# Performance work log

Measured on AMD Instinct MI355X. Metric: run time of the kernel, lower is better.

Reference implementation:

```python
import jax, jax.numpy as jnp
import numpy as np

N_NODES = 200_000
N_EDGES = 6_400_000
N_GRAPHS = 512


def _sage_conv(x, edge_index, Wl, bl, Wr):
    """PyG SAGEConv (mean aggr): lin_l(mean_j x_j) + lin_r(x_i).
    lin_l has bias, lin_r does not. Messages flow src -> dst."""
    src, dst = edge_index[0], edge_index[1]
    n = x.shape[0]
    # gather neighbor features [E, F] and segment-mean into dst nodes
    msg_sum = jax.ops.segment_sum(x[src], dst, num_segments=n)
    deg = jax.ops.segment_sum(jnp.ones((src.shape[0],), x.dtype), dst, num_segments=n)
    mean = msg_sum / jnp.maximum(deg, 1.0)[:, None]  # zero in-degree -> 0
    return mean @ Wl.T + bl + x @ Wr.T


def setup_inputs() -> dict:
    key = jax.random.key(0)
    ks = jax.random.split(key, 9)
    x = jax.random.normal(ks[0], (N_NODES, 1), dtype=jnp.float32)
    edge_index = jax.random.randint(ks[1], (2, N_EDGES), 0, N_NODES, dtype=jnp.int64)
    batch = jnp.sort(jax.random.randint(ks[2], (N_NODES,), 0, N_GRAPHS, dtype=jnp.int64))
    W1l = jax.random.normal(ks[3], (16, 1), dtype=jnp.float32)
    b1 = jax.random.normal(ks[4], (16,), dtype=jnp.float32)
    W1r = jax.random.normal(ks[5], (16, 1), dtype=jnp.float32)
    W2l = jax.random.normal(ks[6], (1, 16), dtype=jnp.float32)
    b2 = jax.random.normal(ks[7], (1,), dtype=jnp.float32)
    W2r = jax.random.normal(ks[8], (1, 16), dtype=jnp.float32)
    return {"x": x, "edge_index": edge_index, "batch": batch, "batch_size": N_GRAPHS,
            "W1l": W1l, "b1": b1, "W1r": W1r, "W2l": W2l, "b2": b2, "W2r": W2r}


def reference(x, edge_index, batch, batch_size, W1l, b1, W1r, W2l, b2, W2r):
    h = _sage_conv(x, edge_index, W1l, b1, W1r)          # [N, 16]
    h = jax.nn.relu(h)
    h = _sage_conv(h, edge_index, W2l, b2, W2r)          # [N, 1]
    # global_add_pool: segment-sum node features by graph id
    out = jax.ops.segment_sum(h, batch, num_segments=batch_size)  # [B, 1]
    return out
```

## Files before the change

### kernel.cpp

```cpp
#include <hip/hip_runtime.h>


#define BLK       1024
#define TILE      (BLK * 4)
#define NBLK      512
#define RING      64
#define NSB       25
#define SBSH      13
#define WMSK      8191u
#define OVFCAP    (1u << 20)
#define CNT_ONE   (1u << 25)
#define FX_BIAS   131072
#define SCALE     4096.0f
#define INV_SCALE (1.0f / 4096.0f)
#define IDQ       8388608.0f

__global__ __launch_bounds__(BLK) void partition_kernel(
    const int* __restrict__ ei, const float* __restrict__ x,
    unsigned* __restrict__ xq1, unsigned* __restrict__ pairs,
    unsigned* __restrict__ blockCnt, unsigned long long* __restrict__ ovf,
    unsigned* __restrict__ ovfTail, int E, int N, int bins, unsigned Mdiv,
    int nc) {
    extern __shared__ unsigned buf[];
    __shared__ unsigned cnt[512];
    const int tid = threadIdx.x;
    const unsigned bid = blockIdx.x;
    for (int j = tid; j < nc; j += BLK) cnt[j] = 0;

    for (int n = (int)bid * BLK + tid; n < N; n += NBLK * BLK)
        xq1[n] = CNT_ONE + (unsigned)((int)rintf(x[n] * SCALE) + FX_BIAS);
    __syncthreads();

    const int ntiles = (E + TILE - 1) / TILE;
    for (int t = (int)bid; t < ntiles; t += NBLK) {
        int e0 = t * TILE + tid * 4;
        int nv = E - e0; nv = nv < 0 ? 0 : (nv > 4 ? 4 : nv);
        int srcv[4], dstv[4];
        if (nv == 4 && ((E & 3) == 0)) {
            int4 s = *(const int4*)(ei + e0);
            int4 d = *(const int4*)(ei + E + e0);
            srcv[0] = s.x; srcv[1] = s.y; srcv[2] = s.z; srcv[3] = s.w;
            dstv[0] = d.x; dstv[1] = d.y; dstv[2] = d.z; dstv[3] = d.w;
        } else {
            for (int j = 0; j < nv; ++j) { srcv[j] = ei[e0 + j]; dstv[j] = ei[E + e0 + j]; }
        }
        for (int j = 0; j < 4; ++j) {
            if (j < nv) {
                unsigned dst = (unsigned)dstv[j];
                unsigned src = (unsigned)srcv[j];
                unsigned pt = (unsigned)(((unsigned long long)dst * Mdiv) >> 32);
                int ld = (int)dst - (int)pt * bins;
                while (ld >= bins) { ld -= bins; ++pt; }
                while (ld < 0)     { ld += bins; --pt; }
                unsigned cell = pt * NSB + (src >> SBSH);
                unsigned w = ((src & WMSK) << 14) | (unsigned)ld;
                unsigned idx = atomicAdd(&cnt[cell], 1u);
                if (idx < RING) {
                    buf[cell * RING + idx] = w;
                } else {
                    unsigned ot = atomicAdd(ovfTail, 1u);
                    if (ot < OVFCAP)
                        ovf[ot] = ((unsigned long long)cell << 32) | w;
                }
            }
        }
    }
    __syncthreads();
    {
        int wv6 = tid >> 6, lane = tid & 63;
        for (int r = wv6; r < nc; r += 16) {
            unsigned len = cnt[r]; if (len > RING) len = RING;
            unsigned* dp = pairs + ((((size_t)r << 9) | bid) << 6);
            for (unsigned jj = lane; jj < len; jj += 64)
                dp[jj] = buf[r * RING + jj];
            if (lane == 0) blockCnt[((size_t)r << 9) | bid] = len;
        }
    }
}

__global__ __launch_bounds__(BLK, 8) void bin1_kernel(
    const unsigned* __restrict__ pairs, const unsigned* __restrict__ blockCnt,
    const unsigned long long* __restrict__ ovf,
    const unsigned* __restrict__ ovfTail,
    const unsigned* __restrict__ xq1, unsigned* __restrict__ slab,
    int N, int bins) {
    extern __shared__ unsigned sm[];
    unsigned* xs = sm;
    unsigned* sb = sm + 8192;
    __shared__ unsigned scnt[NBLK];
    const int tid = threadIdx.x;
    const int cell = blockIdx.x;
    const int p = cell / NSB;
    const int sbk = cell - p * NSB;
    const int wb = sbk << SBSH;
    int nn = N - wb; if (nn > 8192) nn = 8192;
    for (int j = tid; j < nn; j += BLK) xs[j] = xq1[wb + j];
    for (int j = tid; j < bins; j += BLK) sb[j] = 0;
    for (int j = tid; j < NBLK; j += BLK) scnt[j] = blockCnt[((size_t)cell << 9) + j];
    __syncthreads();
    {
        int wv6 = tid >> 6, lane = tid & 63;
        for (int s = wv6; s < NBLK; s += 16) {
            int len = (int)scnt[s];
            const unsigned* sp = pairs + ((((size_t)cell << 9) | (unsigned)s) << 6);
            for (int jj = lane; jj < len; jj += 64) {
                unsigned w = sp[jj];
                atomicAdd(&sb[w & 16383u], xs[w >> 14]);
            }
        }
    }
    {
        unsigned ot = *ovfTail; if (ot > OVFCAP) ot = OVFCAP;
        for (unsigned e = tid; e < ot; e += BLK) {
            unsigned long long pk = ovf[e];
            if ((unsigned)(pk >> 32) == (unsigned)cell) {
                unsigned w = (unsigned)pk;
                atomicAdd(&sb[w & 16383u], xs[w >> 14]);
            }
        }
    }
    __syncthreads();
    unsigned* dst = slab + (size_t)sbk * N + (size_t)p * bins;
    int nb = N - p * bins; if (nb > bins) nb = bins;
    for (int j = tid; j < nb; j += BLK) dst[j] = sb[j];
}

__global__ void node_pass1_kernel(const float* __restrict__ x,
                                  const unsigned* __restrict__ slab,
                                  const float* __restrict__ W1l,
                                  const float* __restrict__ b1,
                                  const float* __restrict__ W1r,
                                  const float* __restrict__ W2l,
                                  const float* __restrict__ W2r,
                                  const float* __restrict__ b2,
                                  const int* __restrict__ batch,
                                  int* __restrict__ pvq,
                                  unsigned* __restrict__ zd,
                                  float* __restrict__ out,
                                  int N) {
    __shared__ float s_w1l[16], s_b1[16], s_w1r[16], s_w2l[16], s_w2r[16];
    if (threadIdx.x < 16) {
        s_w1l[threadIdx.x] = W1l[threadIdx.x];
        s_b1[threadIdx.x]  = b1[threadIdx.x];
        s_w1r[threadIdx.x] = W1r[threadIdx.x];
        s_w2l[threadIdx.x] = W2l[threadIdx.x];
        s_w2r[threadIdx.x] = W2r[threadIdx.x];
    }
    __syncthreads();
    int n = blockIdx.x * blockDim.x + threadIdx.x;
    float b2v = b2[0];
    float val = 0.0f;
    int g;
    if (n < N) {
        unsigned cnt = 0, fx = 0;
#pragma unroll
        for (int c = 0; c < NSB; ++c) {
            unsigned w = slab[(size_t)c * N + n];
            cnt += w >> 25;
            fx  += w & (CNT_ONE - 1);
        }
        float dg  = (float)cnt;
        float sum = (float)(int)(fx - cnt * (unsigned)FX_BIAS) * INV_SCALE;
        float m   = sum / fmaxf(dg, 1.0f);

        float xv = x[n];
        float pa = 0.0f, qa = 0.0f;
#pragma unroll
        for (int f = 0; f < 16; ++f) {
            float h = fmaf(m, s_w1l[f], fmaf(xv, s_w1r[f], s_b1[f]));
            h = fmaxf(h, 0.0f);
            pa = fmaf(h, s_w2l[f], pa);
            qa = fmaf(h, s_w2r[f], qa);
        }
        pvq[n] = (int)rintf(pa * SCALE);
        float invd = 1.0f / fmaxf(dg, 1.0f);
        unsigned q = (unsigned)rintf(invd * IDQ);
        if (q > 8388607u) q = 8388607u;
        g = batch[n];
        zd[n] = ((unsigned)g << 23) | q;
        val = qa + b2v;
    } else {
        g = batch[N - 1];
    }
    int g0 = __shfl(g, 0);
    unsigned long long same = __ballot(g == g0);
    if (same == ~0ULL) {
        for (int off = 32; off > 0; off >>= 1) val += __shfl_down(val, off);
        if ((threadIdx.x & 63) == 0) atomicAdd(&out[g0], val);
    } else {
        atomicAdd(&out[g], val);
    }
}

__global__ __launch_bounds__(BLK, 8) void pool_kernel(
    const unsigned* __restrict__ pairs, const unsigned* __restrict__ blockCnt,
    const unsigned long long* __restrict__ ovf,
    const unsigned* __restrict__ ovfTail,
    const int* __restrict__ pvq, const unsigned* __restrict__ zd,
    unsigned long long* __restrict__ outq,
    int N, int bins) {
    extern __shared__ unsigned sm[];
    int* ps = (int*)sm;
    unsigned* zs = sm + 8192;
    unsigned long long* gbin =
        (unsigned long long*)(sm + 8192 + 10000);
    __shared__ unsigned scnt[NBLK];
    const int tid = threadIdx.x;
    const int cell = blockIdx.x;
    const int p = cell / NSB;
    const int sbk = cell - p * NSB;
    const int wb = sbk << SBSH;
    int nn = N - wb; if (nn > 8192) nn = 8192;
    for (int j = tid; j < nn; j += BLK) ps[j] = pvq[wb + j];
    int nb = N - p * bins; if (nb > bins) nb = bins;
    for (int j = tid; j < nb; j += BLK) zs[j] = zd[(size_t)p * bins + j];
    for (int j = tid; j < NBLK; j += BLK) scnt[j] = blockCnt[((size_t)cell << 9) + j];
    if (tid < 512) gbin[tid] = 0ULL;
    __syncthreads();
    {
        int wv6 = tid >> 6, lane = tid & 63;
        for (int s = wv6; s < NBLK; s += 16) {
            int len = (int)scnt[s];
            const unsigned* sp = pairs + ((((size_t)cell << 9) | (unsigned)s) << 6);
            for (int jj = lane; jj < len; jj += 64) {
                unsigned w = sp[jj];
                unsigned z = zs[w & 16383u];
                int t = (int)rintf((float)ps[w >> 14] *
                                   ((float)(z & 0x7FFFFFu) * (1.0f / IDQ)));
                atomicAdd(&gbin[z >> 23], (unsigned long long)(long long)t);
            }
        }
    }
    {
        unsigned ot = *ovfTail; if (ot > OVFCAP) ot = OVFCAP;
        for (unsigned e = tid; e < ot; e += BLK) {
            unsigned long long pk = ovf[e];
            if ((unsigned)(pk >> 32) == (unsigned)cell) {
                unsigned w = (unsigned)pk;
                unsigned z = zs[w & 16383u];
                int t = (int)rintf((float)ps[w >> 14] *
                                   ((float)(z & 0x7FFFFFu) * (1.0f / IDQ)));
                atomicAdd(&gbin[z >> 23], (unsigned long long)(long long)t);
            }
        }
    }
    __syncthreads();
    if (tid < 512) {
        unsigned long long v = gbin[tid];
        if (v) atomicAdd(&outq[tid], v);
    }
}

__global__ void finalize_kernel(const unsigned long long* __restrict__ outq,
                                float* __restrict__ out, int B) {
    int g = blockIdx.x * blockDim.x + threadIdx.x;
    if (g < B)
        out[g] += (float)(long long)outq[g] * INV_SCALE;
}

extern "C" void kernel_launch(void* const* d_in, const int* in_sizes, int n_in,
                              void* d_out, int out_size, void* d_ws, size_t ws_size,
                              hipStream_t stream) {
    const float* x     = (const float*)d_in[0];
    const int*   ei    = (const int*)d_in[1];
    const int*   batch = (const int*)d_in[2];
    const float* W1l = (const float*)d_in[4];
    const float* b1  = (const float*)d_in[5];
    const float* W1r = (const float*)d_in[6];
    const float* W2l = (const float*)d_in[7];
    const float* b2  = (const float*)d_in[8];
    const float* W2r = (const float*)d_in[9];

    const int N = in_sizes[0];
    const int E = in_sizes[1] / 2;
    float* out = (float*)d_out;

    const int pp   = 20;
    const int bins = (N + pp - 1) / pp;
    const int nc   = pp * NSB;
    const unsigned Mdiv =
        (unsigned)(((1ULL << 32) + (unsigned)bins - 1) / (unsigned)bins);

    unsigned* pairs = (unsigned*)d_ws;
    unsigned* slab1 = pairs + (size_t)nc * NBLK * RING;
    int*      pvq   = (int*)(slab1 + (size_t)NSB * N);
    unsigned* zd    = (unsigned*)(pvq + N);
    unsigned* xq1   = zd + N;
    unsigned* blockCnt = xq1 + N;
    unsigned long long* ovf =
        (unsigned long long*)(blockCnt + (size_t)nc * NBLK);
    unsigned* ovfTail = (unsigned*)(ovf + OVFCAP);
    unsigned long long* outq = (unsigned long long*)(ovfTail + 16);

    hipMemsetAsync(d_out, 0, (size_t)out_size * sizeof(float), stream);
    hipMemsetAsync(ovfTail, 0, (16 + 1024) * sizeof(unsigned), stream);

    const int partShmem = nc * RING * 4;
    const int binShmem  = (8192 + bins) * 4;
    const int poolShmem = (8192 + bins) * 4 + 512 * 8;
    hipFuncSetAttribute((const void*)partition_kernel,
                        hipFuncAttributeMaxDynamicSharedMemorySize, partShmem);
    hipFuncSetAttribute((const void*)bin1_kernel,
                        hipFuncAttributeMaxDynamicSharedMemorySize, binShmem);
    hipFuncSetAttribute((const void*)pool_kernel,
                        hipFuncAttributeMaxDynamicSharedMemorySize, poolShmem);

    const int NB = 256;
    int node_blocks = (N + NB - 1) / NB;

    partition_kernel<<<NBLK, BLK, partShmem, stream>>>(ei, x, xq1, pairs,
                                                       blockCnt, ovf, ovfTail,
                                                       E, N, bins, Mdiv, nc);
    bin1_kernel<<<nc, BLK, binShmem, stream>>>(pairs, blockCnt, ovf, ovfTail,
                                               xq1, slab1, N, bins);
    node_pass1_kernel<<<node_blocks, NB, 0, stream>>>(x, slab1, W1l, b1, W1r,
                                                      W2l, W2r, b2, batch,
                                                      pvq, zd, out, N);
    pool_kernel<<<nc, BLK, poolShmem, stream>>>(pairs, blockCnt, ovf, ovfTail,
                                                pvq, zd, outq, N, bins);
    finalize_kernel<<<(out_size + 255) / 256, 256, 0, stream>>>(outq, out,
                                                                out_size);
}
```

Measured before the change: 201.9 us.

## Merge two source-window cells per block in bin and pool kernels

Each block of the bin1 and pool kernels now handles two adjacent source-node windows (16384 nodes) for the same destination partition instead of one. This halves the grid size and the number of slab partial-sum rows that node_pass1 must read and sum (13 instead of 25), and reuses the destination bin and zd staging across two cells. In exchange each block uses more LDS (about 104 KB for bin1), which lowers occupancy, and each block does twice the serial work. The overflow list is still scanned once per block, so that scan is now repeated half as often.

Result: slower. 246.9 us (+22.3%).

```diff
diff --git a/kernel.cpp b/kernel.cpp
--- a/kernel.cpp
+++ b/kernel.cpp
@@ -6,6 +6,7 @@
 #define NBLK      512
 #define RING      64
 #define NSB       25
+#define NSBH      13
 #define SBSH      13
 #define WMSK      8191u
 #define OVFCAP    (1u << 20)
@@ -86,26 +87,39 @@
     int N, int bins) {
     extern __shared__ unsigned sm[];
     unsigned* xs = sm;
-    unsigned* sb = sm + 8192;
-    __shared__ unsigned scnt[NBLK];
+    unsigned* sb = sm + 16384;
+    __shared__ unsigned scntA[NBLK], scntB[NBLK];
     const int tid = threadIdx.x;
-    const int cell = blockIdx.x;
-    const int p = cell / NSB;
-    const int sbk = cell - p * NSB;
-    const int wb = sbk << SBSH;
-    int nn = N - wb; if (nn > 8192) nn = 8192;
+    const int p = blockIdx.x / NSBH;
+    const int k = blockIdx.x - p * NSBH;
+    const int sbkA = 2 * k;
+    const int sbkB = sbkA + 1;
+    const int cellA = p * NSB + sbkA;
+    const int cellB = cellA + 1;
+    const bool hasB = sbkB < NSB;
+    const int wb = sbkA << SBSH;
+    int nn = N - wb; if (nn > 16384) nn = 16384;
     for (int j = tid; j < nn; j += BLK) xs[j] = xq1[wb + j];
     for (int j = tid; j < bins; j += BLK) sb[j] = 0;
-    for (int j = tid; j < NBLK; j += BLK) scnt[j] = blockCnt[((size_t)cell << 9) + j];
+    for (int j = tid; j < NBLK; j += BLK) {
+        scntA[j] = blockCnt[((size_t)cellA << 9) + j];
+        scntB[j] = hasB ? blockCnt[((size_t)cellB << 9) + j] : 0u;
+    }
     __syncthreads();
     {
         int wv6 = tid >> 6, lane = tid & 63;
         for (int s = wv6; s < NBLK; s += 16) {
-            int len = (int)scnt[s];
-            const unsigned* sp = pairs + ((((size_t)cell << 9) | (unsigned)s) << 6);
-            for (int jj = lane; jj < len; jj += 64) {
-                unsigned w = sp[jj];
+            int lenA = (int)scntA[s];
+            const unsigned* spA = pairs + ((((size_t)cellA << 9) | (unsigned)s) << 6);
+            for (int jj = lane; jj < lenA; jj += 64) {
+                unsigned w = spA[jj];
                 atomicAdd(&sb[w & 16383u], xs[w >> 14]);
+            }
+            int lenB = (int)scntB[s];
+            const unsigned* spB = pairs + ((((size_t)cellB << 9) | (unsigned)s) << 6);
+            for (int jj = lane; jj < lenB; jj += 64) {
+                unsigned w = spB[jj];
+                atomicAdd(&sb[w & 16383u], xs[(w >> 14) + 8192]);
             }
         }
     }
@@ -113,14 +127,18 @@
         unsigned ot = *ovfTail; if (ot > OVFCAP) ot = OVFCAP;
         for (unsigned e = tid; e < ot; e += BLK) {
             unsigned long long pk = ovf[e];
-            if ((unsigned)(pk >> 32) == (unsigned)cell) {
+            unsigned c = (unsigned)(pk >> 32);
+            if (c == (unsigned)cellA) {
                 unsigned w = (unsigned)pk;
                 atomicAdd(&sb[w & 16383u], xs[w >> 14]);
-            }
-        }
-    }
-    __syncthreads();
-    unsigned* dst = slab + (size_t)sbk * N + (size_t)p * bins;
+            } else if (hasB && c == (unsigned)cellB) {
+                unsigned w = (unsigned)pk;
+                atomicAdd(&sb[w & 16383u], xs[(w >> 14) + 8192]);
+            }
+        }
+    }
+    __syncthreads();
+    unsigned* dst = slab + (size_t)k * N + (size_t)p * bins;
     int nb = N - p * bins; if (nb > bins) nb = bins;
     for (int j = tid; j < nb; j += BLK) dst[j] = sb[j];
 }
@@ -154,7 +172,7 @@
     if (n < N) {
         unsigned cnt = 0, fx = 0;
 #pragma unroll
-        for (int c = 0; c < NSB; ++c) {
+        for (int c = 0; c < NSBH; ++c) {
             unsigned w = slab[(size_t)c * N + n];
             cnt += w >> 25;
             fx  += w & (CNT_ONE - 1);
@@ -201,44 +219,62 @@
     int N, int bins) {
     extern __shared__ unsigned sm[];
     int* ps = (int*)sm;
-    unsigned* zs = sm + 8192;
+    unsigned* zs = sm + 16384;
     unsigned long long* gbin =
-        (unsigned long long*)(sm + 8192 + 10000);
-    __shared__ unsigned scnt[NBLK];
+        (unsigned long long*)(sm + 16384 + 10000);
+    __shared__ unsigned scntA[NBLK], scntB[NBLK];
     const int tid = threadIdx.x;
-    const int cell = blockIdx.x;
-    const int p = cell / NSB;
-    const int sbk = cell - p * NSB;
-    const int wb = sbk << SBSH;
-    int nn = N - wb; if (nn > 8192) nn = 8192;
+    const int p = blockIdx.x / NSBH;
+    const int k = blockIdx.x - p * NSBH;
+    const int sbkA = 2 * k;
+    const int sbkB = sbkA + 1;
+    const int cellA = p * NSB + sbkA;
+    const int cellB = cellA + 1;
+    const bool hasB = sbkB < NSB;
+    const int wb = sbkA << SBSH;
+    int nn = N - wb; if (nn > 16384) nn = 16384;
     for (int j = tid; j < nn; j += BLK) ps[j] = pvq[wb + j];
     int nb = N - p * bins; if (nb > bins) nb = bins;
     for (int j = tid; j < nb; j += BLK) zs[j] = zd[(size_t)p * bins + j];
-    for (int j = tid; j < NBLK; j += BLK) scnt[j] = blockCnt[((size_t)cell << 9) + j];
+    for (int j = tid; j < NBLK; j += BLK) {
+        scntA[j] = blockCnt[((size_t)cellA << 9) + j];
+        scntB[j] = hasB ? blockCnt[((size_t)cellB << 9) + j] : 0u;
+    }
     if (tid < 512) gbin[tid] = 0ULL;
     __syncthreads();
     {
         int wv6 = tid >> 6, lane = tid & 63;
         for (int s = wv6; s < NBLK; s += 16) {
-            int len = (int)scnt[s];
-            const unsigned* sp = pairs + ((((size_t)cell << 9) | (unsigned)s) << 6);
-            for (int jj = lane; jj < len; jj += 64) {
-                unsigned w = sp[jj];
+            int lenA = (int)scntA[s];
+            const unsigned* spA = pairs + ((((size_t)cellA << 9) | (unsigned)s) << 6);
+            for (int jj = lane; jj < lenA; jj += 64) {
+                unsigned w = spA[jj];
                 unsigned z = zs[w & 16383u];
                 int t = (int)rintf((float)ps[w >> 14] *
                                    ((float)(z & 0x7FFFFFu) * (1.0f / IDQ)));
                 atomicAdd(&gbin[z >> 23], (unsigned long long)(long long)t);
             }
+            int lenB = (int)scntB[s];
+            const unsigned* spB = pairs + ((((size_t)cellB << 9) | (unsigned)s) << 6);
+            for (int jj = lane; jj < lenB; jj += 64) {
+                unsigned w = spB[jj];
+                unsigned z = zs[w & 16383u];
+                int t = (int)rintf((float)ps[(w >> 14) + 8192] *
+                                   ((float)(z & 0x7FFFFFu) * (1.0f / IDQ)));
+                atomicAdd(&gbin[z >> 23], (unsigned long long)(long long)t);
+            }
         }
     }
     {
         unsigned ot = *ovfTail; if (ot > OVFCAP) ot = OVFCAP;
         for (unsigned e = tid; e < ot; e += BLK) {
             unsigned long long pk = ovf[e];
-            if ((unsigned)(pk >> 32) == (unsigned)cell) {
+            unsigned c = (unsigned)(pk >> 32);
+            if (c == (unsigned)cellA || (hasB && c == (unsigned)cellB)) {
                 unsigned w = (unsigned)pk;
+                int off = (c == (unsigned)cellA) ? 0 : 8192;
                 unsigned z = zs[w & 16383u];
-                int t = (int)rintf((float)ps[w >> 14] *
+                int t = (int)rintf((float)ps[(w >> 14) + off] *
                                    ((float)(z & 0x7FFFFFu) * (1.0f / IDQ)));
                 atomicAdd(&gbin[z >> 23], (unsigned long long)(long long)t);
             }
@@ -283,7 +319,7 @@
 
     unsigned* pairs = (unsigned*)d_ws;
     unsigned* slab1 = pairs + (size_t)nc * NBLK * RING;
-    int*      pvq   = (int*)(slab1 + (size_t)NSB * N);
+    int*      pvq   = (int*)(slab1 + (size_t)NSBH * N);
     unsigned* zd    = (unsigned*)(pvq + N);
     unsigned* xq1   = zd + N;
     unsigned* blockCnt = xq1 + N;
@@ -296,8 +332,8 @@
     hipMemsetAsync(ovfTail, 0, (16 + 1024) * sizeof(unsigned), stream);
 
     const int partShmem = nc * RING * 4;
-    const int binShmem  = (8192 + bins) * 4;
-    const int poolShmem = (8192 + bins) * 4 + 512 * 8;
+    const int binShmem  = (16384 + bins) * 4;
+    const int poolShmem = (16384 + bins) * 4 + 512 * 8;
     hipFuncSetAttribute((const void*)partition_kernel,
                         hipFuncAttributeMaxDynamicSharedMemorySize, partShmem);
     hipFuncSetAttribute((const void*)bin1_kernel,
@@ -307,17 +343,20 @@
 
     const int NB = 256;
     int node_blocks = (N + NB - 1) / NB;
+    const int binGrid = pp * NSBH;
 
     partition_kernel<<<NBLK, BLK, partShmem, stream>>>(ei, x, xq1, pairs,
                                                        blockCnt, ovf, ovfTail,
                                                        E, N, bins, Mdiv, nc);
-    bin1_kernel<<<nc, BLK, binShmem, stream>>>(pairs, blockCnt, ovf, ovfTail,
-                                               xq1, slab1, N, bins);
+    bin1_kernel<<<binGrid, BLK, binShmem, stream>>>(pairs, blockCnt, ovf,
+                                                    ovfTail, xq1, slab1,
+                                                    N, bins);
     node_pass1_kernel<<<node_blocks, NB, 0, stream>>>(x, slab1, W1l, b1, W1r,
                                                       W2l, W2r, b2, batch,
                                                       pvq, zd, out, N);
-    pool_kernel<<<nc, BLK, poolShmem, stream>>>(pairs, blockCnt, ovf, ovfTail,
-                                                pvq, zd, outq, N, bins);
+    pool_kernel<<<binGrid, BLK, poolShmem, stream>>>(pairs, blockCnt, ovf,
+                                                     ovfTail, pvq, zd, outq,
+                                                     N, bins);
     finalize_kernel<<<(out_size + 255) / 256, 256, 0, stream>>>(outq, out,
                                                                 out_size);
 }
```
